# Kernel optimization log

Hardware: AMD Instinct MI355X
Metric: run time of the kernel (lower is better)

Reference implementation:

```python
import jax, jax.numpy as jnp
import numpy as np

HID = 64


def _rev_edges(row, col, n_nodes):
    # Find, for each directed edge (u,v), the index of its reverse (v,u).
    E = row.shape[0]
    keys = row.astype(jnp.int64) * n_nodes + col.astype(jnp.int64)
    rkeys = col.astype(jnp.int64) * n_nodes + row.astype(jnp.int64)
    order = jnp.argsort(keys)
    sk = keys[order]
    pos = jnp.clip(jnp.searchsorted(sk, rkeys), 0, E - 1)
    rev = order[pos]
    has_rev = sk[pos] == rkeys
    return rev, has_rev


def _dmpnn_conv(x, row, col, rev, has_rev, edge_hidden, Wm, bm, Wn, bn):
    # Original semantics: for edge i=(src,tgt), aggregate edge_hidden over all
    # edges j with row[j]==tgt, excluding the reverse edge (tgt,src).
    N = x.shape[0]
    seg = jax.ops.segment_sum(edge_hidden, row, num_segments=N)  # [N,H]
    msg_agg = seg[col] - jnp.where(has_rev[:, None], edge_hidden[rev], 0.0)  # [E,H]
    messages = jax.nn.relu(jnp.concatenate([x[row], msg_agg], axis=-1) @ Wm + bm)  # [E,H]
    node_msg = jax.ops.segment_sum(messages, col, num_segments=N)  # [N,H]
    x_out = jax.nn.relu(jnp.concatenate([x, node_msg], axis=-1) @ Wn + bn)  # [N,H]
    return x_out, messages


def setup_inputs() -> dict:
    key = jax.random.key(0)
    N, E2, B = 40000, 400000, 512  # nodes, undirected edges, graphs
    rng = np.random.default_rng(0)
    a = rng.integers(0, N, E2 * 3)
    b = rng.integers(0, N, E2 * 3)
    m = a != b
    a, b = a[m], b[m]
    canon = np.minimum(a, b).astype(np.int64) * N + np.maximum(a, b)
    _, uidx = np.unique(canon, return_index=True)
    uidx = np.sort(uidx)[:E2]
    a, b = a[uidx], b[uidx]
    row = np.concatenate([a, b]).astype(np.int32)
    col = np.concatenate([b, a]).astype(np.int32)
    edge_index = jnp.asarray(np.stack([row, col]))  # [2, 2*E2], every edge has a reverse
    E = edge_index.shape[1]
    batch = jnp.sort(jax.random.randint(jax.random.fold_in(key, 1), (N,), 0, B, dtype=jnp.int32))
    ks = jax.random.split(jax.random.fold_in(key, 2), 26)
    nrm = lambda k, s: jax.random.normal(k, s, dtype=jnp.float32)
    p = lambda k, s: nrm(k, s) * 0.05
    return {
        "x": nrm(ks[0], (N, 78)),
        "edge_attr": nrm(ks[1], (E, 6)),
        "xt": nrm(ks[2], (B, 128)),
        "edge_index": edge_index,
        "batch": batch,
        "n_graphs": B,
        "We": p(ks[3], (6, HID)), "be": p(ks[4], (HID,)),
        "Wm1": p(ks[5], (78 + HID, HID)), "bm1": p(ks[6], (HID,)),
        "Wn1": p(ks[7], (78 + HID, HID)), "bn1": p(ks[8], (HID,)),
        "Wm2": p(ks[9], (2 * HID, HID)), "bm2": p(ks[10], (HID,)),
        "Wn2": p(ks[11], (2 * HID, HID)), "bn2": p(ks[12], (HID,)),
        "Wm3": p(ks[13], (2 * HID, HID)), "bm3": p(ks[14], (HID,)),
        "Wn3": p(ks[15], (2 * HID, HID)), "bn3": p(ks[16], (HID,)),
        "Wxd": p(ks[17], (HID, 128)), "bxd": p(ks[18], (128,)),
        "W1": p(ks[19], (256, 1024)), "b1": p(ks[20], (1024,)),
        "W2": p(ks[21], (1024, 256)), "b2": p(ks[22], (256,)),
        "Wo": p(ks[23], (256, 1)), "bo": p(ks[24], (1,)),
    }


def reference(x, edge_attr, xt, edge_index, batch, n_graphs, We, be, Wm1, bm1, Wn1, bn1, Wm2, bm2, Wn2, bn2, Wm3, bm3, Wn3, bn3, Wxd, bxd, W1, b1, W2, b2, Wo, bo):
    N = x.shape[0]
    row, col = edge_index[0], edge_index[1]
    rev, has_rev = _rev_edges(row, col, N)
    eh = edge_attr @ We + be  # edge_init
    x1, eh = _dmpnn_conv(x, row, col, rev, has_rev, eh, Wm1, bm1, Wn1, bn1)
    x2, eh = _dmpnn_conv(x1, row, col, rev, has_rev, eh, Wm2, bm2, Wn2, bn2)
    x3, eh = _dmpnn_conv(x2, row, col, rev, has_rev, eh, Wm3, bm3, Wn3, bn3)
    pooled = jax.ops.segment_sum(x3, batch, num_segments=n_graphs)  # global_add_pool
    xg = jax.nn.relu(pooled @ Wxd + bxd)  # [B,128]
    xc = jnp.concatenate([xg, xt], axis=1)  # [B,256]
    h = jax.nn.relu(xc @ W1 + b1)
    h = jax.nn.relu(h @ W2 + b2)
    return h @ Wo + bo  # [B,1]
```

## Files before the change

### kernel.cpp

```cpp
#include <hip/hip_runtime.h>
#include <hip/hip_fp16.h>

using u16 = unsigned short;
using u32 = unsigned int;
using u64 = unsigned long long;

typedef short short8 __attribute__((ext_vector_type(8)));
typedef float f32x4 __attribute__((ext_vector_type(4)));

#define WP_TOP   0
#define WP_BOT   6144
#define WP_NTOP  10240
#define WP_NBOT  16384
#define WP_LAYER 20480

__device__ __forceinline__ float h2f(u16 u){ union{u16 s; _Float16 h;} v; v.s=u; return (float)v.h; }
__device__ __forceinline__ u16 f2h(float f){ union{u16 s; _Float16 h;} v; v.h=(_Float16)f; return v.s; }
__device__ __forceinline__ u32 pack2(float a, float b){ return (u32)f2h(a) | ((u32)f2h(b)<<16); }

__device__ __forceinline__ void store16h(u16* d, const float* a){
  uint4 u0, u1;
  u0.x = pack2(a[0],a[1]);   u0.y = pack2(a[2],a[3]);
  u0.z = pack2(a[4],a[5]);   u0.w = pack2(a[6],a[7]);
  u1.x = pack2(a[8],a[9]);   u1.y = pack2(a[10],a[11]);
  u1.z = pack2(a[12],a[13]); u1.w = pack2(a[14],a[15]);
  *(uint4*)(d)   = u0;
  *(uint4*)(d+8) = u1;
}

__global__ __launch_bounds__(256) void k_deg(
    const int* __restrict__ row, int* __restrict__ cnt, int E)
{
  int e = blockIdx.x*256 + threadIdx.x;
  if (e >= E) return;
  atomicAdd(&cnt[row[e]], 1);
}

__global__ __launch_bounds__(256) void k_bsum(
    const int* __restrict__ cnt, int* __restrict__ bsum, int N)
{
  __shared__ int sh[256];
  int t = threadIdx.x;
  int i = blockIdx.x*256 + t;
  sh[t] = (i < N) ? cnt[i] : 0;
  __syncthreads();
  #pragma unroll
  for (int s=128; s; s>>=1){ if (t<s) sh[t]+=sh[t+s]; __syncthreads(); }
  if (t==0) bsum[blockIdx.x] = sh[0];
}

__global__ __launch_bounds__(256) void k_bscan(
    const int* __restrict__ bsum, int* __restrict__ bofs, int nb,
    int* __restrict__ off, int N)
{
  __shared__ int sh[256];
  int t = threadIdx.x;
  int v = (t < nb) ? bsum[t] : 0;
  sh[t] = v;
  __syncthreads();
  #pragma unroll
  for (int s=1; s<256; s<<=1){
    int u = (t>=s) ? sh[t-s] : 0;
    __syncthreads();
    sh[t] += u;
    __syncthreads();
  }
  if (t < nb) bofs[t] = sh[t] - v;
  if (t == 0) off[N] = sh[nb-1];
}

__global__ __launch_bounds__(256) void k_apply(
    const int* __restrict__ cnt, const int* __restrict__ bofs,
    int* __restrict__ off, int* __restrict__ nxt, int N)
{
  __shared__ int sh[256];
  int t = threadIdx.x;
  int i = blockIdx.x*256 + t;
  int v = (i < N) ? cnt[i] : 0;
  sh[t] = v;
  __syncthreads();
  #pragma unroll
  for (int s=1; s<256; s<<=1){
    int u = (t>=s) ? sh[t-s] : 0;
    __syncthreads();
    sh[t] += u;
    __syncthreads();
  }
  if (i < N){
    int ex = sh[t] - v + bofs[blockIdx.x];
    off[i] = ex;
    nxt[i] = ex;
  }
}

__global__ __launch_bounds__(256) void k_fill(
    const int* __restrict__ row, int* __restrict__ nxt,
    int* __restrict__ perm, int* __restrict__ iperm, int E)
{
  int e = blockIdx.x*256 + threadIdx.x;
  if (e >= E) return;
  int pos = atomicAdd(&nxt[row[e]], 1);
  perm[pos] = e;
  iperm[e] = pos;
}

__global__ __launch_bounds__(256) void k_permarr(
    const int* __restrict__ perm, const int* __restrict__ iperm,
    const int* __restrict__ row, const int* __restrict__ col,
    int* __restrict__ rowp, int* __restrict__ colp, int* __restrict__ revp,
    int E, int E2)
{
  int i = blockIdx.x*256 + threadIdx.x;
  if (i >= E) return;
  int e = perm[i];
  rowp[i] = row[e];
  colp[i] = col[e];
  int re = (e < E2) ? e + E2 : e - E2;
  revp[i] = iperm[re];
}

__global__ __launch_bounds__(256) void k_xconv(
    const float* __restrict__ x, u16* __restrict__ xh, int N)
{
  int t = blockIdx.x*256 + threadIdx.x;
  if (t >= N*96) return;
  int n = t / 96, k = t - n*96;
  xh[t] = (k < 78) ? f2h(x[(size_t)n*78 + k]) : (u16)0;
}

__global__ __launch_bounds__(256) void k_edge_init(
    const float* __restrict__ ea, const int* __restrict__ iperm,
    const float* __restrict__ We, const float* __restrict__ be,
    u16* __restrict__ eh, int E)
{
  int tid = blockIdx.x*256 + threadIdx.x;
  int e = tid >> 2;
  if (e >= E) return;
  int t = tid & 3;
  int slot = iperm[e];
  const float* a = ea + (size_t)e*6;
  float acc[16];
  #pragma unroll
  for (int j=0;j<16;j++) acc[j] = be[t*16+j];
  #pragma unroll
  for (int k=0;k<6;k++){
    float av = a[k];
    const float* w = We + k*64 + t*16;
    #pragma unroll
    for (int j=0;j<16;j++) acc[j] += av*w[j];
  }
  store16h(eh + ((size_t)slot<<6) + t*16, acc);
}

__global__ __launch_bounds__(256) void k_seg0(
    const float* __restrict__ ea, const int* __restrict__ perm,
    const int* __restrict__ off, const float* __restrict__ We,
    const float* __restrict__ be, u16* __restrict__ segb, int N)
{
  int w = (blockIdx.x << 2) + (threadIdx.x >> 6);
  if (w >= N) return;
  int lane = threadIdx.x & 63;
  int lo = off[w], hi = off[w+1];
  float wcol[6];
  #pragma unroll
  for (int k=0;k<6;k++) wcol[k] = We[k*64 + lane];
  float es[6] = {0.f,0.f,0.f,0.f,0.f,0.f};
  for (int j = lo; j < hi; j++){
    int e = perm[j];
    const float* a = ea + (size_t)e*6;
    #pragma unroll
    for (int k=0;k<6;k++) es[k] += a[k];
  }
  float acc = (float)(hi - lo) * be[lane];
  #pragma unroll
  for (int k=0;k<6;k++) acc += es[k]*wcol[k];
  segb[((size_t)w<<6) + lane] = f2h(acc);
}

__global__ __launch_bounds__(256) void k_prepw(
    const float* __restrict__ Wm, const float* __restrict__ Wn,
    int XD, int KT, u16* __restrict__ dst)
{
  int t = blockIdx.x*256 + threadIdx.x;
  int topFL = KT*256;
  const float* W; int rbase, rvalid, dofs, fl;
  if (t < topFL)                   { W = Wm; rbase = 0;  rvalid = XD; dofs = WP_TOP;  fl = t; }
  else if (t < topFL+512)          { W = Wm; rbase = XD; rvalid = 64; dofs = WP_BOT;  fl = t - topFL; }
  else if (t < 2*topFL+512)        { W = Wn; rbase = 0;  rvalid = XD; dofs = WP_NTOP; fl = t - topFL - 512; }
  else if (t < 2*topFL+1024)       { W = Wn; rbase = XD; rvalid = 64; dofs = WP_NBOT; fl = t - 2*topFL - 512; }
  else return;
  int f = fl >> 6, lane = fl & 63;
  int nt = f & 3, kk = f >> 2;
  int n = (nt<<4) + (lane & 15);
  int krel = (kk<<5) + ((lane>>4)<<3);
  u16* d = dst + dofs + (size_t)f*512 + lane*8;
  #pragma unroll
  for (int j=0;j<8;j++){
    int kr = krel + j;
    d[j] = (kr < rvalid) ? f2h(W[(size_t)(rbase+kr)*64 + n]) : (u16)0;
  }
}

__global__ __launch_bounds__(256) void k_packw(
    const float* __restrict__ W, int K, int Nout, u16* __restrict__ dst)
{
  int t = blockIdx.x*256 + threadIdx.x;
  int NT = Nout >> 4;
  int total = (K >> 5) * NT * 64;
  if (t >= total) return;
  int f = t >> 6, lane = t & 63;
  int nt = f % NT, kk = f / NT;
  int n = (nt<<4) + (lane & 15);
  int kb = (kk<<5) + ((lane>>4)<<3);
  u16* d = dst + ((size_t)f*64 + lane)*8;
  #pragma unroll
  for (int j=0;j<8;j++) d[j] = f2h(W[(size_t)(kb+j)*Nout + n]);
}

__global__ __launch_bounds__(256) void k_gemm(
    const u16* __restrict__ A, int lda, const u16* __restrict__ BP,
    const float* __restrict__ bias, void* __restrict__ outv, int ldo,
    int M, int NT, int KT, int dorelu, int oh16)
{
  int lane = threadIdx.x & 63;
  int wid = (blockIdx.x << 2) + (threadIdx.x >> 6);
  int nb = NT >> 2;
  int mblk = wid / nb, nblk = wid - mblk*nb;
  int m0 = mblk << 4;
  if (m0 >= M) return;
  int n0 = nblk << 6;
  int nlo = lane & 15;
  int khi = (lane >> 4) << 3;
  int r0 = m0 + nlo; if (r0 > M-1) r0 = M-1;

  f32x4 acc[4];
  #pragma unroll
  for (int nt=0;nt<4;nt++){ f32x4 z = {0.f,0.f,0.f,0.f}; acc[nt]=z; }
  for (int kk=0; kk<KT; kk++){
    short8 a = *(const short8*)(A + (size_t)r0*lda + (kk<<5) + khi);
    #pragma unroll
    for (int nt=0;nt<4;nt++){
      short8 b = *(const short8*)(BP + ((size_t)(kk*NT + (nblk<<2) + nt)*64 + lane)*8);
      acc[nt] = __builtin_amdgcn_mfma_f32_16x16x32_f16(a, b, acc[nt], 0,0,0);
    }
  }
  int mrow = (lane >> 4) << 2;
  #pragma unroll
  for (int r=0;r<4;r++){
    int m = m0 + mrow + r;
    if (m >= M) continue;
    #pragma unroll
    for (int nt=0;nt<4;nt++){
      float v = acc[nt][r] + bias[n0 + (nt<<4) + nlo];
      if (dorelu) v = fmaxf(v, 0.f);
      if (oh16) ((u16*)outv)[(size_t)m*ldo + n0 + (nt<<4) + nlo] = f2h(v);
      else      ((float*)outv)[(size_t)m*ldo + n0 + (nt<<4) + nlo] = v;
    }
  }
}

template<int KT>
__global__ __launch_bounds__(256) void k_proj(
    const u16* __restrict__ xin, const u16* __restrict__ segb,
    const u16* __restrict__ wp, const float* __restrict__ bm,
    u16* __restrict__ pxb, u16* __restrict__ psb, int N)
{
  int lane = threadIdx.x & 63;
  int wid = (blockIdx.x << 2) + (threadIdx.x >> 6);
  int base = wid << 4;
  if (base >= N) return;
  int nlo = lane & 15;
  int khi = (lane >> 4) << 3;

  short8 bt[KT][4];
  #pragma unroll
  for (int kk=0;kk<KT;kk++)
    #pragma unroll
    for (int nt=0;nt<4;nt++)
      bt[kk][nt] = *(const short8*)(wp + WP_TOP + ((size_t)((kk<<2)|nt)*64 + lane)*8);
  short8 bb[2][4];
  #pragma unroll
  for (int kk=0;kk<2;kk++)
    #pragma unroll
    for (int nt=0;nt<4;nt++)
      bb[kk][nt] = *(const short8*)(wp + WP_BOT + ((size_t)((kk<<2)|nt)*64 + lane)*8);

  int r0 = base + nlo; if (r0 > N-1) r0 = N-1;
  const u16* xrow = xin + (size_t)r0*(KT*32);
  short8 ax[KT];
  #pragma unroll
  for (int kk=0;kk<KT;kk++) ax[kk] = *(const short8*)(xrow + (kk<<5) + khi);
  const u16* srow = segb + ((size_t)r0<<6);
  short8 as[2];
  #pragma unroll
  for (int kk=0;kk<2;kk++) as[kk] = *(const short8*)(srow + (kk<<5) + khi);

  f32x4 accP[4], accS[4];
  #pragma unroll
  for (int nt=0;nt<4;nt++){ f32x4 z = {0.f,0.f,0.f,0.f}; accP[nt]=z; accS[nt]=z; }
  #pragma unroll
  for (int kk=0;kk<KT;kk++)
    #pragma unroll
    for (int nt=0;nt<4;nt++)
      accP[nt] = __builtin_amdgcn_mfma_f32_16x16x32_f16(ax[kk], bt[kk][nt], accP[nt], 0,0,0);
  #pragma unroll
  for (int kk=0;kk<2;kk++)
    #pragma unroll
    for (int nt=0;nt<4;nt++)
      accS[nt] = __builtin_amdgcn_mfma_f32_16x16x32_f16(as[kk], bb[kk][nt], accS[nt], 0,0,0);

  float bmv[4];
  #pragma unroll
  for (int nt=0;nt<4;nt++) bmv[nt] = bm[(nt<<4) + nlo];

  int mrow = (lane >> 4) << 2;
  #pragma unroll
  for (int r=0;r<4;r++){
    int node = base + mrow + r;
    if (node >= N) continue;
    #pragma unroll
    for (int nt=0;nt<4;nt++){
      pxb[((size_t)node<<6) + (nt<<4) + nlo] = f2h(accP[nt][r] + bmv[nt]);
      psb[((size_t)node<<6) + (nt<<4) + nlo] = f2h(accS[nt][r]);
    }
  }
}

__global__ __launch_bounds__(256) void k_scatmfma(
    const u16* __restrict__ eh, const u16* __restrict__ wp,
    const u16* __restrict__ pxb, const u16* __restrict__ psb,
    const int* __restrict__ rowp, const int* __restrict__ colp,
    const int* __restrict__ revp, u16* __restrict__ msg, int E)
{
  int lane = threadIdx.x & 63;
  int wid = (blockIdx.x << 2) + (threadIdx.x >> 6);
  int base = wid << 4;
  if (base >= E) return;
  int nlo = lane & 15;
  int khi = (lane >> 4) << 3;

  short8 bb[2][4];
  #pragma unroll
  for (int kk=0;kk<2;kk++)
    #pragma unroll
    for (int nt=0;nt<4;nt++)
      bb[kk][nt] = *(const short8*)(wp + WP_BOT + ((size_t)((kk<<2)|nt)*64 + lane)*8);

  int sa = base + nlo; if (sa > E-1) sa = E-1;
  const u16* ehp = eh + ((size_t)sa<<6) + khi;
  short8 a0 = *(const short8*)(ehp);
  short8 a1 = *(const short8*)(ehp + 32);

  f32x4 acc[4];
  #pragma unroll
  for (int nt=0;nt<4;nt++){
    f32x4 z = {0.f,0.f,0.f,0.f};
    acc[nt] = z;
    acc[nt] = __builtin_amdgcn_mfma_f32_16x16x32_f16(a0, bb[0][nt], acc[nt], 0,0,0);
    acc[nt] = __builtin_amdgcn_mfma_f32_16x16x32_f16(a1, bb[1][nt], acc[nt], 0,0,0);
  }

  int mrow = (lane >> 4) << 2;
  #pragma unroll
  for (int r=0;r<4;r++){
    int slot = base + mrow + r;
    if (slot >= E) continue;
    int rp = rowp[slot];
    int cp = colp[slot];
    int rv = revp[slot];
    const u16* pr = psb + ((size_t)rp<<6) + nlo;
    const u16* pc = pxb + ((size_t)cp<<6) + nlo;
    u16* ob = msg + ((size_t)rv<<6) + nlo;
    #pragma unroll
    for (int nt=0;nt<4;nt++){
      float v = h2f(pc[nt<<4]) + h2f(pr[nt<<4]) - acc[nt][r];
      ob[nt<<4] = f2h(fmaxf(v, 0.f));
    }
  }
}

__global__ __launch_bounds__(256) void k_gnmsg(
    const u16* __restrict__ msg, const int* __restrict__ revp,
    const int* __restrict__ off, u16* __restrict__ nmsgb,
    u16* __restrict__ segnext, int N)
{
  int w = (blockIdx.x << 2) + (threadIdx.x >> 6);
  if (w >= N) return;
  int lane = threadIdx.x & 63;
  int g = lane >> 4, l = lane & 15;
  int lo = off[w], hi = off[w+1];
  float s0=0.f,s1=0.f,s2=0.f,s3=0.f;
  float t0=0.f,t1=0.f,t2=0.f,t3=0.f;
  if (segnext){
    for (int j = lo + g; j < hi; j += 4){
      int i = revp[j];
      uint2 v = *(const uint2*)(msg + ((size_t)i<<6) + (l<<2));
      uint2 u = *(const uint2*)(msg + ((size_t)j<<6) + (l<<2));
      s0 += h2f((u16)v.x); s1 += h2f((u16)(v.x>>16)); s2 += h2f((u16)v.y); s3 += h2f((u16)(v.y>>16));
      t0 += h2f((u16)u.x); t1 += h2f((u16)(u.x>>16)); t2 += h2f((u16)u.y); t3 += h2f((u16)(u.y>>16));
    }
  } else {
    for (int j = lo + g; j < hi; j += 4){
      int i = revp[j];
      uint2 v = *(const uint2*)(msg + ((size_t)i<<6) + (l<<2));
      s0 += h2f((u16)v.x); s1 += h2f((u16)(v.x>>16)); s2 += h2f((u16)v.y); s3 += h2f((u16)(v.y>>16));
    }
  }
  s0 += __shfl_xor(s0,16,64); s0 += __shfl_xor(s0,32,64);
  s1 += __shfl_xor(s1,16,64); s1 += __shfl_xor(s1,32,64);
  s2 += __shfl_xor(s2,16,64); s2 += __shfl_xor(s2,32,64);
  s3 += __shfl_xor(s3,16,64); s3 += __shfl_xor(s3,32,64);
  if (segnext){
    t0 += __shfl_xor(t0,16,64); t0 += __shfl_xor(t0,32,64);
    t1 += __shfl_xor(t1,16,64); t1 += __shfl_xor(t1,32,64);
    t2 += __shfl_xor(t2,16,64); t2 += __shfl_xor(t2,32,64);
    t3 += __shfl_xor(t3,16,64); t3 += __shfl_xor(t3,32,64);
  }
  if (g == 0){
    uint2 o; o.x = pack2(s0,s1); o.y = pack2(s2,s3);
    *(uint2*)(nmsgb + ((size_t)w<<6) + (l<<2)) = o;
    if (segnext){
      uint2 q; q.x = pack2(t0,t1); q.y = pack2(t2,t3);
      *(uint2*)(segnext + ((size_t)w<<6) + (l<<2)) = q;
    }
  }
}

template<int KT>
__global__ __launch_bounds__(256) void k_nodef(
    const u16* __restrict__ xin, const u16* __restrict__ nmsgb,
    const u16* __restrict__ wp, const float* __restrict__ bn,
    u16* __restrict__ xout, int N)
{
  int lane = threadIdx.x & 63;
  int wid = (blockIdx.x << 2) + (threadIdx.x >> 6);
  int base = wid << 4;
  if (base >= N) return;
  int nlo = lane & 15;
  int khi = (lane >> 4) << 3;

  short8 bt[KT][4];
  #pragma unroll
  for (int kk=0;kk<KT;kk++)
    #pragma unroll
    for (int nt=0;nt<4;nt++)
      bt[kk][nt] = *(const short8*)(wp + WP_NTOP + ((size_t)((kk<<2)|nt)*64 + lane)*8);
  short8 bb[2][4];
  #pragma unroll
  for (int kk=0;kk<2;kk++)
    #pragma unroll
    for (int nt=0;nt<4;nt++)
      bb[kk][nt] = *(const short8*)(wp + WP_NBOT + ((size_t)((kk<<2)|nt)*64 + lane)*8);

  int r0 = base + nlo; if (r0 > N-1) r0 = N-1;
  const u16* xrow = xin + (size_t)r0*(KT*32);
  short8 ax[KT];
  #pragma unroll
  for (int kk=0;kk<KT;kk++) ax[kk] = *(const short8*)(xrow + (kk<<5) + khi);
  const u16* mrp = nmsgb + ((size_t)r0<<6);
  short8 am[2];
  #pragma unroll
  for (int kk=0;kk<2;kk++) am[kk] = *(const short8*)(mrp + (kk<<5) + khi);

  f32x4 acc[4];
  #pragma unroll
  for (int nt=0;nt<4;nt++){ f32x4 z = {0.f,0.f,0.f,0.f}; acc[nt]=z; }
  #pragma unroll
  for (int kk=0;kk<KT;kk++)
    #pragma unroll
    for (int nt=0;nt<4;nt++)
      acc[nt] = __builtin_amdgcn_mfma_f32_16x16x32_f16(ax[kk], bt[kk][nt], acc[nt], 0,0,0);
  #pragma unroll
  for (int kk=0;kk<2;kk++)
    #pragma unroll
    for (int nt=0;nt<4;nt++)
      acc[nt] = __builtin_amdgcn_mfma_f32_16x16x32_f16(am[kk], bb[kk][nt], acc[nt], 0,0,0);

  float bnv[4];
  #pragma unroll
  for (int nt=0;nt<4;nt++) bnv[nt] = bn[(nt<<4) + nlo];

  int mrow = (lane >> 4) << 2;
  #pragma unroll
  for (int r=0;r<4;r++){
    int node = base + mrow + r;
    if (node >= N) continue;
    #pragma unroll
    for (int nt=0;nt<4;nt++)
      xout[((size_t)node<<6) + (nt<<4) + nlo] = f2h(fmaxf(acc[nt][r] + bnv[nt], 0.f));
  }
}

__global__ __launch_bounds__(256) void k_goff(
    const int* __restrict__ batch, int* __restrict__ goff, int N, int B)
{
  int n = blockIdx.x*256 + threadIdx.x;
  if (n >= N) return;
  int bcur = batch[n];
  int bprev = (n == 0) ? -1 : batch[n-1];
  for (int g = bprev + 1; g <= bcur; ++g) goff[g] = n;
  if (n == N-1) { for (int g = bcur + 1; g <= B; ++g) goff[g] = N; }
}

__global__ __launch_bounds__(256) void k_pool(
    const u16* __restrict__ xin, const int* __restrict__ goff,
    u16* __restrict__ pooledh, int B)
{
  int g = (blockIdx.x << 2) + (threadIdx.x >> 6);
  if (g >= B) return;
  int lane = threadIdx.x & 63;
  int lo = goff[g], hi = goff[g + 1];
  float s = 0.f;
  for (int n = lo; n < hi; n++) s += h2f(xin[((size_t)n << 6) + lane]);
  pooledh[((size_t)g << 6) + lane] = f2h(s);
}

__global__ __launch_bounds__(256) void k_xtconv(
    const float* __restrict__ xt, u16* __restrict__ ab1, int B)
{
  int t = blockIdx.x*256 + threadIdx.x;
  if (t >= B*128) return;
  int r = t >> 7, c = t & 127;
  ab1[(size_t)r*256 + 128 + c] = f2h(xt[t]);
}

__global__ __launch_bounds__(256) void k_out(
    const float* __restrict__ h2, const float* __restrict__ Wo,
    const float* __restrict__ bo, float* __restrict__ out, int B)
{
  int w = (blockIdx.x << 2) + (threadIdx.x >> 6);
  if (w >= B) return;
  int lane = threadIdx.x & 63;
  const float* h = h2 + (size_t)w*256;
  float s = 0.f;
  #pragma unroll
  for (int k=0;k<4;k++) s += h[lane + (k<<6)] * Wo[lane + (k<<6)];
  #pragma unroll
  for (int off=32; off; off>>=1) s += __shfl_down(s, off, 64);
  if (lane == 0) out[w] = s + bo[0];
}

extern "C" void kernel_launch(void* const* d_in, const int* in_sizes, int n_in,
                              void* d_out, int out_size, void* d_ws, size_t ws_size,
                              hipStream_t stream)
{
  const float* x    = (const float*)d_in[0];
  const float* ea   = (const float*)d_in[1];
  const float* xt   = (const float*)d_in[2];
  const int*   eidx = (const int*)d_in[3];
  const int*   batch= (const int*)d_in[4];
  const float* We   = (const float*)d_in[6];
  const float* be   = (const float*)d_in[7];
  const float* Wm[3]= {(const float*)d_in[8],  (const float*)d_in[12], (const float*)d_in[16]};
  const float* bm[3]= {(const float*)d_in[9],  (const float*)d_in[13], (const float*)d_in[17]};
  const float* Wn[3]= {(const float*)d_in[10], (const float*)d_in[14], (const float*)d_in[18]};
  const float* bn[3]= {(const float*)d_in[11], (const float*)d_in[15], (const float*)d_in[19]};
  const float* Wxd  = (const float*)d_in[20];
  const float* bxd  = (const float*)d_in[21];
  const float* W1   = (const float*)d_in[22];
  const float* b1   = (const float*)d_in[23];
  const float* W2   = (const float*)d_in[24];
  const float* b2   = (const float*)d_in[25];
  const float* Wo   = (const float*)d_in[26];
  const float* bo   = (const float*)d_in[27];

  const int N = in_sizes[0] / 78;
  const int E = in_sizes[1] / 6;
  const int B = in_sizes[2] / 128;
  const int E2 = E / 2;
  const int* row = eidx;
  const int* col = eidx + E;

  char* p = (char*)d_ws;
  size_t off = 0;
  auto alloc = [&](size_t b)->void* {
    void* r = p + off;
    off = (off + b + 255) & ~(size_t)255;
    return r;
  };
  u16*   ehA   = (u16*)  alloc((size_t)E * 128);
  u16*   ehB   = (u16*)  alloc((size_t)E * 128);
  int*   rowp  = (int*)  alloc((size_t)E * 4);
  int*   colp  = (int*)  alloc((size_t)E * 4);
  int*   revp  = (int*)  alloc((size_t)E * 4);
  int*   offs  = (int*)  alloc((size_t)(N+1) * 4);
  u16*   xh    = (u16*)  alloc((size_t)N * 192);
  u16*   sA    = (u16*)  alloc((size_t)N * 128);
  u16*   sB    = (u16*)  alloc((size_t)N * 128);
  u16*   pxb   = (u16*)  alloc((size_t)N * 128);
  u16*   psb   = (u16*)  alloc((size_t)N * 128);
  u16*   xa    = (u16*)  alloc((size_t)N * 128);
  u16*   xb    = (u16*)  alloc((size_t)N * 128);
  int*   goff  = (int*)  alloc((size_t)(B+1) * 4);
  u16*   pooledh=(u16*)  alloc((size_t)B * 128);
  u16*   ab1   = (u16*)  alloc((size_t)B * 512);
  u16*   h1h   = (u16*)  alloc((size_t)B * 2048);
  float* h2f   = (float*)alloc((size_t)B * 1024);
  u16*   wpack = (u16*)  alloc((size_t)3 * WP_LAYER * 2);
  u16*   wxdP  = (u16*)  alloc((size_t)(64/32)*(128/16)*512 * 2);
  u16*   w1P   = (u16*)  alloc((size_t)(256/32)*(1024/16)*512 * 2);
  u16*   w2P   = (u16*)  alloc((size_t)(1024/32)*(256/16)*512 * 2);

  char* ehBc = (char*)ehB;
  int* perm  = (int*)ehBc;
  int* iperm = perm + E;
  int* cnt   = iperm + E;
  int* nxt   = cnt + N;
  int* bsum  = nxt + N;
  int* bofs  = bsum + 1024;

  dim3 blk(256);
  int gE   = (E + 255) / 256;
  int gE4  = ((size_t)E*4 + 255) / 256;
  int gEm  = (E + 63) / 64;
  int gN   = (N + 255) / 256;
  int gNm  = (N + 63) / 64;
  int gNw  = (N + 3) / 4;
  int gBw  = (B + 3) / 4;
  int gXc  = (N*96 + 255) / 256;
  int nb   = (N + 255) / 256;

  hipMemsetAsync(cnt, 0, (size_t)N * 4, stream);
  k_deg  <<<gE, blk, 0, stream>>>(row, cnt, E);
  k_bsum <<<nb, blk, 0, stream>>>(cnt, bsum, N);
  k_bscan<<<1,  blk, 0, stream>>>(bsum, bofs, nb, offs, N);
  k_apply<<<nb, blk, 0, stream>>>(cnt, bofs, offs, nxt, N);
  k_fill <<<gE, blk, 0, stream>>>(row, nxt, perm, iperm, E);
  k_permarr<<<gE, blk, 0, stream>>>(perm, iperm, row, col, rowp, colp, revp, E, E2);
  k_edge_init<<<gE4, blk, 0, stream>>>(ea, iperm, We, be, ehA, E);
  k_seg0<<<gNw, blk, 0, stream>>>(ea, perm, offs, We, be, sA, N);
  k_xconv<<<gXc, blk, 0, stream>>>(x, xh, N);
  k_goff<<<gN, blk, 0, stream>>>(batch, goff, N, B);
  for (int L = 0; L < 3; ++L) {
    int XD = (L == 0) ? 78 : 64;
    int KT = (L == 0) ? 3 : 2;
    k_prepw<<<10, blk, 0, stream>>>(Wm[L], Wn[L], XD, KT, wpack + (size_t)L*WP_LAYER);
  }
  k_packw<<<(1024 + 255)/256, blk, 0, stream>>>(Wxd, 64, 128, wxdP);
  k_packw<<<(32768 + 255)/256, blk, 0, stream>>>(W1, 256, 1024, w1P);
  k_packw<<<(32768 + 255)/256, blk, 0, stream>>>(W2, 1024, 256, w2P);

  const u16* ehin = ehA;
  u16* ehout = ehB;
  const u16* xin = xh;
  u16* segcur = sA;
  u16* segnxt = sB;
  for (int L = 0; L < 3; ++L) {
    u16* xout = (L % 2 == 0) ? xa : xb;
    const u16* wp = wpack + (size_t)L*WP_LAYER;
    if (L == 0) k_proj<3><<<gNm, blk, 0, stream>>>(xin, segcur, wp, bm[L], pxb, psb, N);
    else        k_proj<2><<<gNm, blk, 0, stream>>>(xin, segcur, wp, bm[L], pxb, psb, N);
    k_scatmfma<<<gEm, blk, 0, stream>>>(ehin, wp, pxb, psb, rowp, colp, revp, ehout, E);
    k_gnmsg<<<gNw, blk, 0, stream>>>(ehout, revp, offs, pxb, (L < 2) ? segnxt : (u16*)nullptr, N);
    if (L == 0) k_nodef<3><<<gNm, blk, 0, stream>>>(xin, pxb, wp, bn[L], xout, N);
    else        k_nodef<2><<<gNm, blk, 0, stream>>>(xin, pxb, wp, bn[L], xout, N);
    u16* tmp = (u16*)ehin; ehin = ehout; ehout = tmp;
    u16* ts = segcur; segcur = segnxt; segnxt = ts;
    xin = xout;
  }

  k_pool<<<gBw, blk, 0, stream>>>(xa, goff, pooledh, B);
  k_xtconv<<<(B*128 + 255)/256, blk, 0, stream>>>(xt, ab1, B);
  {
    int waves = ((B + 15)/16) * (128/64);
    k_gemm<<<(waves + 3)/4, blk, 0, stream>>>(pooledh, 64, wxdP, bxd, ab1, 256, B, 128>>4, 64>>5, 1, 1);
  }
  {
    int waves = ((B + 15)/16) * (1024/64);
    k_gemm<<<(waves + 3)/4, blk, 0, stream>>>(ab1, 256, w1P, b1, h1h, 1024, B, 1024>>4, 256>>5, 1, 1);
  }
  {
    int waves = ((B + 15)/16) * (256/64);
    k_gemm<<<(waves + 3)/4, blk, 0, stream>>>(h1h, 1024, w2P, b2, h2f, 256, B, 256>>4, 1024>>5, 1, 0);
  }
  k_out<<<gBw, blk, 0, stream>>>(h2f, Wo, bo, (float*)d_out, B);
}
```

Baseline: 728.9 us.

## Fold edge-init linear into layer-0 message weights and skip materializing edge hidden

Layer 0 no longer writes the initial edge hidden state to memory and runs the MFMA scatter over it. The edge-init weights and bias are pre-multiplied with the bottom half of the layer-0 message weight (We·Wm_bot, be·Wm_bot) into a small fused matrix. The new k_scat0 kernel computes each edge's reverse-edge term directly from the 6 raw edge attributes. This removes one full E×64 write and read plus the layer-0 MFMA pass. In exchange it does a per-edge gather of the raw attributes through perm, and the pre-multiplied products change rounding slightly.

```diff
diff --git a/kernel.cpp b/kernel.cpp
--- a/kernel.cpp
+++ b/kernel.cpp
@@ -28,6 +28,19 @@
   *(uint4*)(d+8) = u1;
 }
 
+__device__ __forceinline__ void load16h(const u16* p, float* out){
+  uint4 v0 = *(const uint4*)(p);
+  uint4 v1 = *(const uint4*)(p+8);
+  out[0]=h2f((u16)v0.x);  out[1]=h2f((u16)(v0.x>>16));
+  out[2]=h2f((u16)v0.y);  out[3]=h2f((u16)(v0.y>>16));
+  out[4]=h2f((u16)v0.z);  out[5]=h2f((u16)(v0.z>>16));
+  out[6]=h2f((u16)v0.w);  out[7]=h2f((u16)(v0.w>>16));
+  out[8]=h2f((u16)v1.x);  out[9]=h2f((u16)(v1.x>>16));
+  out[10]=h2f((u16)v1.y); out[11]=h2f((u16)(v1.y>>16));
+  out[12]=h2f((u16)v1.z); out[13]=h2f((u16)(v1.z>>16));
+  out[14]=h2f((u16)v1.w); out[15]=h2f((u16)(v1.w>>16));
+}
+
 __global__ __launch_bounds__(256) void k_deg(
     const int* __restrict__ row, int* __restrict__ cnt, int E)
 {
@@ -128,30 +141,6 @@
   xh[t] = (k < 78) ? f2h(x[(size_t)n*78 + k]) : (u16)0;
 }
 
-__global__ __launch_bounds__(256) void k_edge_init(
-    const float* __restrict__ ea, const int* __restrict__ iperm,
-    const float* __restrict__ We, const float* __restrict__ be,
-    u16* __restrict__ eh, int E)
-{
-  int tid = blockIdx.x*256 + threadIdx.x;
-  int e = tid >> 2;
-  if (e >= E) return;
-  int t = tid & 3;
-  int slot = iperm[e];
-  const float* a = ea + (size_t)e*6;
-  float acc[16];
-  #pragma unroll
-  for (int j=0;j<16;j++) acc[j] = be[t*16+j];
-  #pragma unroll
-  for (int k=0;k<6;k++){
-    float av = a[k];
-    const float* w = We + k*64 + t*16;
-    #pragma unroll
-    for (int j=0;j<16;j++) acc[j] += av*w[j];
-  }
-  store16h(eh + ((size_t)slot<<6) + t*16, acc);
-}
-
 __global__ __launch_bounds__(256) void k_seg0(
     const float* __restrict__ ea, const int* __restrict__ perm,
     const int* __restrict__ off, const float* __restrict__ We,
@@ -175,6 +164,22 @@
   #pragma unroll
   for (int k=0;k<6;k++) acc += es[k]*wcol[k];
   segb[((size_t)w<<6) + lane] = f2h(acc);
+}
+
+__global__ __launch_bounds__(256) void k_fusew(
+    const float* __restrict__ We, const float* __restrict__ be,
+    const float* __restrict__ Wb, float* __restrict__ wf)
+{
+  int t = blockIdx.x*256 + threadIdx.x;
+  if (t >= 448) return;
+  int k = t >> 6, n = t & 63;
+  float s = 0.f;
+  if (k < 6) {
+    for (int j=0;j<64;j++) s += We[k*64 + j] * Wb[(size_t)j*64 + n];
+  } else {
+    for (int j=0;j<64;j++) s += be[j] * Wb[(size_t)j*64 + n];
+  }
+  wf[t] = s;
 }
 
 __global__ __launch_bounds__(256) void k_prepw(
@@ -324,6 +329,44 @@
       psb[((size_t)node<<6) + (nt<<4) + nlo] = f2h(accS[nt][r]);
     }
   }
+}
+
+__global__ __launch_bounds__(256) void k_scat0(
+    const float* __restrict__ ea, const int* __restrict__ perm,
+    const float* __restrict__ wf,
+    const u16* __restrict__ pxb, const u16* __restrict__ psb,
+    const int* __restrict__ rowp, const int* __restrict__ colp,
+    const int* __restrict__ revp, u16* __restrict__ msg, int E)
+{
+  int tid = blockIdx.x*256 + threadIdx.x;
+  int i = tid >> 2;
+  if (i >= E) return;
+  int t = tid & 3;
+  int e  = perm[i];
+  int rp = rowp[i];
+  int cp = colp[i];
+  int rv = revp[i];
+  const float* a = ea + (size_t)e*6;
+  float av[6];
+  #pragma unroll
+  for (int k=0;k<6;k++) av[k] = a[k];
+  float proj[16];
+  const float* bp = wf + 384 + t*16;
+  #pragma unroll
+  for (int j=0;j<16;j++) proj[j] = bp[j];
+  #pragma unroll
+  for (int k=0;k<6;k++){
+    const float* w = wf + k*64 + t*16;
+    #pragma unroll
+    for (int j=0;j<16;j++) proj[j] += av[k]*w[j];
+  }
+  float pc[16], pr[16];
+  load16h(pxb + ((size_t)cp<<6) + t*16, pc);
+  load16h(psb + ((size_t)rp<<6) + t*16, pr);
+  float val[16];
+  #pragma unroll
+  for (int j=0;j<16;j++) val[j] = fmaxf(pc[j] + pr[j] - proj[j], 0.f);
+  store16h(msg + ((size_t)rv<<6) + t*16, val);
 }
 
 __global__ __launch_bounds__(256) void k_scatmfma(
@@ -595,14 +638,15 @@
   u16*   pooledh=(u16*)  alloc((size_t)B * 128);
   u16*   ab1   = (u16*)  alloc((size_t)B * 512);
   u16*   h1h   = (u16*)  alloc((size_t)B * 2048);
-  float* h2f   = (float*)alloc((size_t)B * 1024);
+  float* h2f_  = (float*)alloc((size_t)B * 1024);
   u16*   wpack = (u16*)  alloc((size_t)3 * WP_LAYER * 2);
   u16*   wxdP  = (u16*)  alloc((size_t)(64/32)*(128/16)*512 * 2);
   u16*   w1P   = (u16*)  alloc((size_t)(256/32)*(1024/16)*512 * 2);
   u16*   w2P   = (u16*)  alloc((size_t)(1024/32)*(256/16)*512 * 2);
-
-  char* ehBc = (char*)ehB;
-  int* perm  = (int*)ehBc;
+  float* wfuse = (float*)alloc((size_t)448 * 4);
+
+  char* ehAc = (char*)ehA;
+  int* perm  = (int*)ehAc;
   int* iperm = perm + E;
   int* cnt   = iperm + E;
   int* nxt   = cnt + N;
@@ -627,10 +671,10 @@
   k_apply<<<nb, blk, 0, stream>>>(cnt, bofs, offs, nxt, N);
   k_fill <<<gE, blk, 0, stream>>>(row, nxt, perm, iperm, E);
   k_permarr<<<gE, blk, 0, stream>>>(perm, iperm, row, col, rowp, colp, revp, E, E2);
-  k_edge_init<<<gE4, blk, 0, stream>>>(ea, iperm, We, be, ehA, E);
   k_seg0<<<gNw, blk, 0, stream>>>(ea, perm, offs, We, be, sA, N);
   k_xconv<<<gXc, blk, 0, stream>>>(x, xh, N);
   k_goff<<<gN, blk, 0, stream>>>(batch, goff, N, B);
+  k_fusew<<<2, blk, 0, stream>>>(We, be, Wm[0] + (size_t)78*64, wfuse);
   for (int L = 0; L < 3; ++L) {
     int XD = (L == 0) ? 78 : 64;
     int KT = (L == 0) ? 3 : 2;
@@ -640,24 +684,22 @@
   k_packw<<<(32768 + 255)/256, blk, 0, stream>>>(W1, 256, 1024, w1P);
   k_packw<<<(32768 + 255)/256, blk, 0, stream>>>(W2, 1024, 256, w2P);
 
-  const u16* ehin = ehA;
-  u16* ehout = ehB;
-  const u16* xin = xh;
-  u16* segcur = sA;
-  u16* segnxt = sB;
-  for (int L = 0; L < 3; ++L) {
-    u16* xout = (L % 2 == 0) ? xa : xb;
-    const u16* wp = wpack + (size_t)L*WP_LAYER;
-    if (L == 0) k_proj<3><<<gNm, blk, 0, stream>>>(xin, segcur, wp, bm[L], pxb, psb, N);
-    else        k_proj<2><<<gNm, blk, 0, stream>>>(xin, segcur, wp, bm[L], pxb, psb, N);
-    k_scatmfma<<<gEm, blk, 0, stream>>>(ehin, wp, pxb, psb, rowp, colp, revp, ehout, E);
-    k_gnmsg<<<gNw, blk, 0, stream>>>(ehout, revp, offs, pxb, (L < 2) ? segnxt : (u16*)nullptr, N);
-    if (L == 0) k_nodef<3><<<gNm, blk, 0, stream>>>(xin, pxb, wp, bn[L], xout, N);
-    else        k_nodef<2><<<gNm, blk, 0, stream>>>(xin, pxb, wp, bn[L], xout, N);
-    u16* tmp = (u16*)ehin; ehin = ehout; ehout = tmp;
-    u16* ts = segcur; segcur = segnxt; segnxt = ts;
-    xin = xout;
-  }
+  const u16* wp0 = wpack;
+  const u16* wp1 = wpack + (size_t)WP_LAYER;
+  const u16* wp2 = wpack + (size_t)2*WP_LAYER;
+
+  k_proj<3><<<gNm, blk, 0, stream>>>(xh, sA, wp0, bm[0], pxb, psb, N);
+  k_scat0<<<gE4, blk, 0, stream>>>(ea, perm, wfuse, pxb, psb, rowp, colp, revp, ehB, E);
+  k_gnmsg<<<gNw, blk, 0, stream>>>(ehB, revp, offs, pxb, sB, N);
+  k_nodef<3><<<gNm, blk, 0, stream>>>(xh, pxb, wp0, bn[0], xa, N);
+  k_proj<2><<<gNm, blk, 0, stream>>>(xa, sB, wp1, bm[1], pxb, psb, N);
+  k_scatmfma<<<gEm, blk, 0, stream>>>(ehB, wp1, pxb, psb, rowp, colp, revp, ehA, E);
+  k_gnmsg<<<gNw, blk, 0, stream>>>(ehA, revp, offs, pxb, sA, N);
+  k_nodef<2><<<gNm, blk, 0, stream>>>(xa, pxb, wp1, bn[1], xb, N);
+  k_proj<2><<<gNm, blk, 0, stream>>>(xb, sA, wp2, bm[2], pxb, psb, N);
+  k_scatmfma<<<gEm, blk, 0, stream>>>(ehA, wp2, pxb, psb, rowp, colp, revp, ehB, E);
+  k_gnmsg<<<gNw, blk, 0, stream>>>(ehB, revp, offs, pxb, (u16*)nullptr, N);
+  k_nodef<2><<<gNm, blk, 0, stream>>>(xb, pxb, wp2, bn[2], xa, N);
 
   k_pool<<<gBw, blk, 0, stream>>>(xa, goff, pooledh, B);
   k_xtconv<<<(B*128 + 255)/256, blk, 0, stream>>>(xt, ab1, B);
@@ -671,7 +713,7 @@
   }
   {
     int waves = ((B + 15)/16) * (256/64);
-    k_gemm<<<(waves + 3)/4, blk, 0, stream>>>(h1h, 1024, w2P, b2, h2f, 256, B, 256>>4, 1024>>5, 1, 0);
-  }
-  k_out<<<gBw, blk, 0, stream>>>(h2f, Wo, bo, (float*)d_out, B);
-}
+    k_gemm<<<(waves + 3)/4, blk, 0, stream>>>(h1h, 1024, w2P, b2, h2f_, 256, B, 256>>4, 1024>>5, 1, 0);
+  }
+  k_out<<<gBw, blk, 0, stream>>>(h2f_, Wo, bo, (float*)d_out, B);
+}
```

New measurement: 677.4 us. -7.1%, faster.
